# Kernel optimization log

Hardware: AMD Instinct MI355X
Metric: run time of the kernel (lower is better)

The kernel has to match this reference:

```python
import jax, jax.numpy as jnp
from jax import lax
import numpy as np

B, H, W, D_MODEL = 2, 64, 64, 192
D_INNER, D_STATE, DT_RANK = 384, 16, 12
L = H * W
LN_EPS = 1e-5


def setup_inputs() -> dict:
    ks = jax.random.split(jax.random.key(0), 12)
    rng = np.random.default_rng(0)
    perm = rng.permutation(L).astype(np.int32)

    def p(i, shape, scale=0.02):
        return jax.random.normal(ks[i], shape, dtype=jnp.float32) * scale

    return {
        "x": jax.random.normal(ks[0], (B, H, W, D_MODEL), dtype=jnp.float32),
        "condition": jax.random.normal(ks[1], (B, H, W, D_MODEL), dtype=jnp.float32),
        "W_in": p(2, (2 * D_INNER, D_MODEL)),
        "W_con": p(3, (D_INNER, D_MODEL)),
        "conv_w": p(4, (D_INNER, 1, 3, 3)),
        "conv_b": jnp.zeros((D_INNER,), jnp.float32),
        "con_conv_w": p(5, (D_INNER, 1, 3, 3)),
        "con_conv_b": jnp.zeros((D_INNER,), jnp.float32),
        "x_proj_w": p(6, (DT_RANK + 2 * D_STATE, D_INNER)),
        "dt_proj_w": p(7, (D_INNER, DT_RANK)),
        "dt_proj_b": p(8, (D_INNER,), 0.1),
        "A_logs": jnp.tile(jnp.log(jnp.arange(1, D_STATE + 1, dtype=jnp.float32))[None, :], (D_INNER, 1)),
        "Ds": jnp.ones((D_INNER,), jnp.float32),
        "ln_w": jnp.ones((D_INNER,), jnp.float32),
        "ln_b": jnp.zeros((D_INNER,), jnp.float32),
        "W_out": p(9, (D_MODEL, D_INNER)),
        "scan_path": jnp.asarray(perm),
        "rev_scan_path": jnp.asarray(np.argsort(perm).astype(np.int32)),
    }


def _dwconv(x, w, b):
    # depthwise 3x3 conv, SAME padding; x: [B, C, H, W], w: [C, 1, 3, 3]
    y = lax.conv_general_dilated(x, w, (1, 1), "SAME",
                                 dimension_numbers=("NCHW", "OIHW", "NCHW"),
                                 feature_group_count=x.shape[1])
    return y + b[None, :, None, None]


def _selective_scan(u, delta, A, Bs, Cs, D):
    # u, delta: [B, D, L]; A: [D, N]; Bs, Cs: [B, N, L]; D: [D]
    dA = jnp.exp(jnp.einsum("bdl,dn->lbdn", delta, A))          # [L, B, D, N]
    dBu = jnp.einsum("bdl,bnl,bdl->lbdn", delta, Bs, u)          # [L, B, D, N]
    Ct = jnp.transpose(Cs, (2, 0, 1))                             # [L, B, N]
    h0 = jnp.zeros(dA.shape[1:], dA.dtype)

    def step(h, inp):
        a, b, c = inp
        h = a * h + b
        return h, jnp.einsum("bdn,bn->bd", h, c)

    _, ys = lax.scan(step, h0, (dA, dBu, Ct))                     # ys: [L, B, D]
    y = jnp.transpose(ys, (1, 2, 0))                              # [B, D, L]
    return y + u * D[None, :, None]


def _forward(x, condition, W_in, W_con, conv_w, conv_b, con_conv_w, con_conv_b,
             x_proj_w, dt_proj_w, dt_proj_b, A_logs, Ds, ln_w, ln_b, W_out,
             scan_path, rev_scan_path):
    b, h, w, _ = x.shape
    l = h * w
    xz = x @ W_in.T                                               # [B, H, W, 2*Din]
    xa, z = jnp.split(xz, 2, axis=-1)
    z = jax.nn.silu(z)
    c = condition @ W_con.T
    xa = jax.nn.silu(_dwconv(jnp.transpose(xa, (0, 3, 1, 2)), conv_w, conv_b))
    c = jax.nn.silu(_dwconv(jnp.transpose(c, (0, 3, 1, 2)), con_conv_w, con_conv_b))
    d = xa.shape[1]
    xs = xa.reshape(b, d, l)[:, :, scan_path]                     # forward_permutation, K=1
    cs = c.reshape(b, d, l)[:, :, scan_path]
    x_dbl = jnp.einsum("bdl,cd->bcl", xs + cs, x_proj_w)          # [B, R+2N, L]
    r, n = dt_proj_w.shape[1], A_logs.shape[1]
    dts = jnp.einsum("brl,dr->bdl", x_dbl[:, :r], dt_proj_w)
    Bs = x_dbl[:, r:r + n]
    Cs = x_dbl[:, r + n:]
    A = -jnp.exp(A_logs)
    delta = jax.nn.softplus(dts + dt_proj_b[None, :, None])       # delta_softplus=True
    y = _selective_scan(xs, delta, A, Bs, Cs, Ds)                 # [B, D, L]
    y = y[:, :, rev_scan_path]                                    # backward_permutation
    y = jnp.transpose(y, (0, 2, 1))                               # [B, L, D]
    mu = jnp.mean(y, axis=-1, keepdims=True)
    var = jnp.var(y, axis=-1, keepdims=True)
    y = (y - mu) * lax.rsqrt(var + LN_EPS) * ln_w + ln_b          # out_norm
    y = y.reshape(b, h, w, d) * z
    return y @ W_out.T                                            # out_proj (no bias)


def reference(x, condition, W_in, W_con, conv_w, conv_b, con_conv_w, con_conv_b,
              x_proj_w, dt_proj_w, dt_proj_b, A_logs, Ds, ln_w, ln_b, W_out,
              scan_path, rev_scan_path):
    return _forward(x, condition, W_in, W_con, conv_w, conv_b, con_conv_w,
                    con_conv_b, x_proj_w, dt_proj_w, dt_proj_b, A_logs, Ds,
                    ln_w, ln_b, W_out, scan_path, rev_scan_path)
```

## Files before the change

kernel.cpp:

```cpp
#include <hip/hip_runtime.h>
#include <math.h>

#define BB 2
#define HH 64
#define WW 64
#define DM 192
#define DI 384
#define NS 16
#define DTR 12
#define LL 4096
#define ROWS (BB*LL)
#define NCHUNK 64
#define LCHUNK 64
#define NCOMB 448

typedef __attribute__((ext_vector_type(8))) short bf16x8;
typedef __attribute__((ext_vector_type(4))) float f32x4;

__device__ __forceinline__ float silu_f(float v) {
    return v / (1.0f + __expf(-v));
}

__device__ __forceinline__ unsigned short f2bf(float f) {
    union { float f; unsigned int u; } c; c.f = f;
    unsigned int u = c.u;
    u += 0x7fffu + ((u >> 16) & 1u);
    return (unsigned short)(u >> 16);
}

__device__ __forceinline__ bf16x8 f2bf8(float4 a, float4 b) {
    bf16x8 r;
    r[0] = (short)f2bf(a.x); r[1] = (short)f2bf(a.y);
    r[2] = (short)f2bf(a.z); r[3] = (short)f2bf(a.w);
    r[4] = (short)f2bf(b.x); r[5] = (short)f2bf(b.y);
    r[6] = (short)f2bf(b.z); r[7] = (short)f2bf(b.w);
    return r;
}

__global__ __launch_bounds__(256) void prep_weights(
    const float* __restrict__ w_in, const float* __restrict__ w_con,
    const float* __restrict__ w_out,
    const float* __restrict__ x_proj_w, const float* __restrict__ dt_w,
    unsigned short* __restrict__ w_in_bf, unsigned short* __restrict__ w_con_bf,
    unsigned short* __restrict__ w_out_bf, unsigned short* __restrict__ wc)
{
    int idx = blockIdx.x * 256 + threadIdx.x;
    if (idx < 73728) {
        const float4* src; ushort4* dst; int off;
        if (idx < 36864)      { src = (const float4*)w_in;  dst = (ushort4*)w_in_bf;  off = idx; }
        else if (idx < 55296) { src = (const float4*)w_con; dst = (ushort4*)w_con_bf; off = idx - 36864; }
        else                  { src = (const float4*)w_out; dst = (ushort4*)w_out_bf; off = idx - 55296; }
        float4 v = src[off];
        ushort4 o;
        o.x = f2bf(v.x); o.y = f2bf(v.y); o.z = f2bf(v.z); o.w = f2bf(v.w);
        dst[off] = o;
    } else {
        int e = idx - 73728;
        if (e >= NCOMB * DI) return;
        int row = e / DI, k = e - row * DI;
        float v = 0.f;
        if (row < 384) {
            const float* dw = dt_w + row * DTR;
            #pragma unroll
            for (int r = 0; r < DTR; ++r) v += dw[r] * x_proj_w[r * DI + k];
        } else if (row < 416) {
            v = x_proj_w[(12 + (row - 384)) * DI + k];
        }
        wc[e] = f2bf(v);
    }
}

__device__ __forceinline__ void gemm_epilogue(
    int mode, int row, int col, int N, float v,
    const float* __restrict__ bias,
    float* __restrict__ out0, float* __restrict__ out1)
{
    if (mode == 0) {
        if (col < 384) out0[(size_t)row * 384 + col] = v;
        else           out1[(size_t)row * 384 + (col - 384)] = silu_f(v);
    } else if (mode == 1) {
        out0[(size_t)row * N + col] = v;
    } else {
        if (col < 384) {
            float a = v + bias[col];
            out0[(size_t)row * 384 + col] = (a > 20.f) ? a : log1pf(__expf(a));
        } else if (col < 416) {
            int idx = col - 384;
            int pos = (idx < 16) ? ((idx & 7) * 4 + (idx >> 3))
                                 : (((idx - 16) & 7) * 4 + 2 + ((idx - 16) >> 3));
            out1[(size_t)row * 32 + pos] = v;
        }
    }
}

__global__ __launch_bounds__(256) void gemm_bf16(
    const unsigned short* __restrict__ A, const unsigned short* __restrict__ W,
    const float* __restrict__ bias,
    float* __restrict__ out0, float* __restrict__ out1,
    int M, int N, int K, int mode)
{
    __shared__ __align__(16) unsigned short sA[64 * 40];
    __shared__ __align__(16) unsigned short sB[64 * 40];
    const int bm = blockIdx.x * 64;
    const int bn = blockIdx.y * 64;
    const int tid  = threadIdx.x;
    const int wave = tid >> 6;
    const int lane = tid & 63;
    const int quad = lane >> 4;
    const int l16  = lane & 15;
    const int lrow = tid >> 2;
    const int lkof = (tid & 3) * 8;

    f32x4 acc[4];
    #pragma unroll
    for (int t = 0; t < 4; ++t) acc[t] = (f32x4)(0.f);

    const int arow = (wave * 16 + l16) * 40 + quad * 8;

    for (int k0 = 0; k0 < K; k0 += 32) {
        *(bf16x8*)&sA[lrow * 40 + lkof] =
            *(const bf16x8*)&A[(size_t)(bm + lrow) * K + k0 + lkof];
        *(bf16x8*)&sB[lrow * 40 + lkof] =
            *(const bf16x8*)&W[(size_t)(bn + lrow) * K + k0 + lkof];
        __syncthreads();
        bf16x8 a = *(bf16x8*)&sA[arow];
        #pragma unroll
        for (int t = 0; t < 4; ++t) {
            bf16x8 b = *(bf16x8*)&sB[(t * 16 + l16) * 40 + quad * 8];
            acc[t] = __builtin_amdgcn_mfma_f32_16x16x32_bf16(a, b, acc[t], 0, 0, 0);
        }
        __syncthreads();
    }

    #pragma unroll
    for (int t = 0; t < 4; ++t) {
        int col = bn + t * 16 + l16;
        #pragma unroll
        for (int r = 0; r < 4; ++r) {
            int row = bm + wave * 16 + quad * 4 + r;
            gemm_epilogue(mode, row, col, N, acc[t][r], bias, out0, out1);
        }
    }
}

__global__ __launch_bounds__(256) void gemm_dual(
    const float* __restrict__ x, const float* __restrict__ cond,
    const unsigned short* __restrict__ w_in_bf,
    const unsigned short* __restrict__ w_con_bf,
    float* __restrict__ xa_pre, float* __restrict__ z_silu,
    float* __restrict__ c_pre)
{
    const int zz = blockIdx.z;
    if (zz == 1 && blockIdx.y >= 6) return;
    const float* A = zz ? cond : x;
    const unsigned short* W = zz ? w_con_bf : w_in_bf;
    float* out0 = zz ? c_pre : xa_pre;
    float* out1 = z_silu;
    const int mode = zz ? 1 : 0;
    const int N = zz ? 384 : 768;

    __shared__ __align__(16) unsigned short sA[64 * 40];
    __shared__ __align__(16) unsigned short sB[64 * 40];
    const int bm = blockIdx.x * 64;
    const int bn = blockIdx.y * 64;
    const int tid  = threadIdx.x;
    const int wave = tid >> 6;
    const int lane = tid & 63;
    const int quad = lane >> 4;
    const int l16  = lane & 15;
    const int lrow = tid >> 2;
    const int lkof = (tid & 3) * 8;

    f32x4 acc[4];
    #pragma unroll
    for (int t = 0; t < 4; ++t) acc[t] = (f32x4)(0.f);

    const int arow = (wave * 16 + l16) * 40 + quad * 8;

    for (int k0 = 0; k0 < DM; k0 += 32) {
        const float* ap = &A[(size_t)(bm + lrow) * DM + k0 + lkof];
        float4 a0 = *(const float4*)ap;
        float4 a1 = *(const float4*)(ap + 4);
        *(bf16x8*)&sA[lrow * 40 + lkof] = f2bf8(a0, a1);
        *(bf16x8*)&sB[lrow * 40 + lkof] =
            *(const bf16x8*)&W[(size_t)(bn + lrow) * DM + k0 + lkof];
        __syncthreads();
        bf16x8 a = *(bf16x8*)&sA[arow];
        #pragma unroll
        for (int t = 0; t < 4; ++t) {
            bf16x8 b = *(bf16x8*)&sB[(t * 16 + l16) * 40 + quad * 8];
            acc[t] = __builtin_amdgcn_mfma_f32_16x16x32_bf16(a, b, acc[t], 0, 0, 0);
        }
        __syncthreads();
    }

    #pragma unroll
    for (int t = 0; t < 4; ++t) {
        int col = bn + t * 16 + l16;
        #pragma unroll
        for (int r = 0; r < 4; ++r) {
            int row = bm + wave * 16 + quad * 4 + r;
            gemm_epilogue(mode, row, col, N, acc[t][r], nullptr, out0, out1);
        }
    }
}

__global__ __launch_bounds__(256) void dwconv2_scatter(
    const float* __restrict__ xin, const float* __restrict__ cin,
    const float* __restrict__ wx, const float* __restrict__ bx,
    const float* __restrict__ wc, const float* __restrict__ bc,
    const int* __restrict__ rev_scan_path,
    float* __restrict__ xs_buf, unsigned short* __restrict__ s_bf)
{
    const int tile = blockIdx.x;
    const int c0   = blockIdx.y * 64;
    const int b    = blockIdx.z;
    const int h0 = (tile >> 3) * 8, w0 = (tile & 7) * 8;
    __shared__ float smx[10 * 10 * 64];
    __shared__ float smc[10 * 10 * 64];
    __shared__ int   jtile[64];

    for (int idx = threadIdx.x; idx < 6400; idx += 256) {
        int pix = idx >> 6, ch = idx & 63;
        int py = pix / 10, px = pix - py * 10;
        int gh = h0 + py - 1, gw = w0 + px - 1;
        float vx = 0.f, vc = 0.f;
        if (gh >= 0 && gh < 64 && gw >= 0 && gw < 64) {
            size_t g = ((size_t)(b * LL + gh * 64 + gw)) * DI + c0 + ch;
            vx = xin[g]; vc = cin[g];
        }
        smx[idx] = vx; smc[idx] = vc;
    }
    if (threadIdx.x < 64) {
        int l = (h0 + (threadIdx.x >> 3)) * 64 + (w0 + (threadIdx.x & 7));
        jtile[threadIdx.x] = rev_scan_path[l];
    }
    __syncthreads();

    const int ch = threadIdx.x & 63;
    const int pq = threadIdx.x >> 6;
    float wrx[9], wrc[9];
    #pragma unroll
    for (int k = 0; k < 9; ++k) {
        wrx[k] = wx[(c0 + ch) * 9 + k];
        wrc[k] = wc[(c0 + ch) * 9 + k];
    }
    const float bvx = bx[c0 + ch];
    const float bvc = bc[c0 + ch];

    #pragma unroll
    for (int i = 0; i < 16; ++i) {
        int p  = pq * 16 + i;
        int ph = p >> 3, pw = p & 7;
        float ax = bvx, ac = bvc;
        #pragma unroll
        for (int ki = 0; ki < 3; ++ki)
            #pragma unroll
            for (int kj = 0; kj < 3; ++kj) {
                int si = ((ph + ki) * 10 + (pw + kj)) * 64 + ch;
                ax += wrx[ki * 3 + kj] * smx[si];
                ac += wrc[ki * 3 + kj] * smc[si];
            }
        float xv = silu_f(ax);
        float sv = xv + silu_f(ac);
        size_t o = ((size_t)(b * LL + jtile[p])) * DI + c0 + ch;
        xs_buf[o] = xv;
        s_bf[o]   = f2bf(sv);
    }
}

__global__ __launch_bounds__(256) void scan_chunkA(
    const float* __restrict__ xs, const float* __restrict__ delta,
    const float* __restrict__ btct, const float* __restrict__ A_logs,
    float* __restrict__ chunkA, float* __restrict__ chunkB)
{
    const int c = blockIdx.x;
    const int g = blockIdx.y;
    const int b = blockIdx.z;
    const int t = threadIdx.x;
    const int grp = t >> 3, p = t & 7;
    const int d = g * 32 + grp;
    const float Av0 = -__expf(A_logs[d * NS + p]);
    const float Av1 = -__expf(A_logs[d * NS + p + 8]);
    const int j0 = c * LCHUNK;

    const float*  dl = delta + ((size_t)b * LL + j0) * DI + d;
    const float*  ul = xs    + ((size_t)b * LL + j0) * DI + d;
    const float2* bl = (const float2*)btct + ((size_t)b * LL + j0) * 16 + p * 2;

    float h0 = 0.f, h1 = 0.f, Sd = 0.f;
    float dv[4], uv[4]; float2 bv[4];
    #pragma unroll
    for (int q = 0; q < 4; ++q) {
        dv[q] = dl[(size_t)q * DI]; uv[q] = ul[(size_t)q * DI]; bv[q] = bl[(size_t)q * 16];
    }
    for (int j = 0; j < LCHUNK; j += 4) {
        float nd[4], nu[4]; float2 nb[4];
        if (j + 4 < LCHUNK) {
            #pragma unroll
            for (int q = 0; q < 4; ++q) {
                int jj = j + 4 + q;
                nd[q] = dl[(size_t)jj * DI]; nu[q] = ul[(size_t)jj * DI]; nb[q] = bl[(size_t)jj * 16];
            }
        }
        #pragma unroll
        for (int q = 0; q < 4; ++q) {
            float e0 = __expf(dv[q] * Av0);
            float e1 = __expf(dv[q] * Av1);
            float du = dv[q] * uv[q];
            h0 = e0 * h0 + bv[q].x * du;
            h1 = e1 * h1 + bv[q].y * du;
            Sd += dv[q];
        }
        #pragma unroll
        for (int q = 0; q < 4; ++q) { dv[q]=nd[q]; uv[q]=nu[q]; bv[q]=nb[q]; }
    }
    size_t idx = (((size_t)b * DI + d) * 8 + p) * NCHUNK + c;
    ((float2*)chunkA)[idx] = make_float2(__expf(Sd * Av0), __expf(Sd * Av1));
    ((float2*)chunkB)[idx] = make_float2(h0, h1);
}

__global__ __launch_bounds__(256) void scan_combine(
    const float* __restrict__ chunkA, const float* __restrict__ chunkB,
    float* __restrict__ hstart)
{
    const int gid = blockIdx.x * 256 + threadIdx.x;
    const float2* A2 = (const float2*)chunkA + (size_t)gid * NCHUNK;
    const float2* B2 = (const float2*)chunkB + (size_t)gid * NCHUNK;
    float2*       H2 = (float2*)hstart       + (size_t)gid * NCHUNK;
    float h0 = 0.f, h1 = 0.f;
    for (int c = 0; c < NCHUNK; ++c) {
        float2 a = A2[c], bv = B2[c];
        H2[c] = make_float2(h0, h1);
        h0 = a.x * h0 + bv.x;
        h1 = a.y * h1 + bv.y;
    }
}

__global__ __launch_bounds__(256) void scan_chunkC(
    const float* __restrict__ xs, const float* __restrict__ delta,
    const float* __restrict__ btct,
    const float* __restrict__ A_logs, const float* __restrict__ Ds,
    const float* __restrict__ hstart,
    float* __restrict__ yt)
{
    const int c = blockIdx.x;
    const int g = blockIdx.y;
    const int b = blockIdx.z;
    const int t = threadIdx.x;
    const int grp = t >> 3, p = t & 7;
    const int d = g * 32 + grp;
    const float Av0 = -__expf(A_logs[d * NS + p]);
    const float Av1 = -__expf(A_logs[d * NS + p + 8]);
    const float Dv = Ds[d];
    const int j0 = c * LCHUNK;

    const float*  dl  = delta + ((size_t)b * LL + j0) * DI + d;
    const float*  ul  = xs    + ((size_t)b * LL + j0) * DI + d;
    const float4* bcl = (const float4*)btct + ((size_t)b * LL + j0) * 8 + p;
    float* yl = yt + ((size_t)b * LL + j0) * DI + d;

    float2 h = ((const float2*)hstart)[(((size_t)b * DI + d) * 8 + p) * NCHUNK + c];
    float h0 = h.x, h1 = h.y;

    float dv[4], uv[4]; float4 bc[4];
    #pragma unroll
    for (int q = 0; q < 4; ++q) {
        dv[q] = dl[(size_t)q * DI]; uv[q] = ul[(size_t)q * DI]; bc[q] = bcl[(size_t)q * 8];
    }
    for (int j = 0; j < LCHUNK; j += 4) {
        float nd[4], nu[4]; float4 nbc[4];
        if (j + 4 < LCHUNK) {
            #pragma unroll
            for (int q = 0; q < 4; ++q) {
                int jj = j + 4 + q;
                nd[q] = dl[(size_t)jj * DI]; nu[q] = ul[(size_t)jj * DI]; nbc[q] = bcl[(size_t)jj * 8];
            }
        }
        #pragma unroll
        for (int q = 0; q < 4; ++q) {
            float e0 = __expf(dv[q] * Av0);
            float e1 = __expf(dv[q] * Av1);
            float du = dv[q] * uv[q];
            h0 = e0 * h0 + bc[q].x * du;
            h1 = e1 * h1 + bc[q].y * du;
            float acc = h0 * bc[q].z + h1 * bc[q].w;
            acc += __shfl_xor(acc, 4, 8);
            acc += __shfl_xor(acc, 2, 8);
            acc += __shfl_xor(acc, 1, 8);
            if (p == 0) yl[(size_t)(j + q) * DI] = acc + uv[q] * Dv;
        }
        #pragma unroll
        for (int q = 0; q < 4; ++q) { dv[q]=nd[q]; uv[q]=nu[q]; bc[q]=nbc[q]; }
    }
}

__global__ __launch_bounds__(256) void ln_gemm(
    const float* __restrict__ yt, const float* __restrict__ z,
    const int* __restrict__ rev_path,
    const float* __restrict__ ln_w, const float* __restrict__ ln_b,
    const unsigned short* __restrict__ w_out_bf,
    float* __restrict__ out)
{
    __shared__ __align__(16) unsigned short sA[32 * 392];
    __shared__ __align__(16) unsigned short sB[192 * 40];
    const int l0 = blockIdx.x * 32;
    const int tid  = threadIdx.x;
    const int wave = tid >> 6;
    const int lane = tid & 63;

    for (int r = wave; r < 32; r += 4) {
        int gl = l0 + r;
        int b = gl >> 12;
        int pos = gl & (LL - 1);
        int j = b * LL + rev_path[pos];
        const float* yrow = yt + (size_t)j * DI;
        float v[6];
        float s = 0.f, s2 = 0.f;
        #pragma unroll
        for (int i = 0; i < 6; ++i) {
            v[i] = yrow[lane + 64 * i];
            s += v[i]; s2 += v[i] * v[i];
        }
        #pragma unroll
        for (int off = 32; off > 0; off >>= 1) {
            s  += __shfl_xor(s, off);
            s2 += __shfl_xor(s2, off);
        }
        float mu  = s * (1.0f / DI);
        float var = s2 * (1.0f / DI) - mu * mu;
        float inv = rsqrtf(var + 1e-5f);
        const float* zrow = z + (size_t)gl * DI;
        #pragma unroll
        for (int i = 0; i < 6; ++i) {
            int cidx = lane + 64 * i;
            float val = ((v[i] - mu) * inv * ln_w[cidx] + ln_b[cidx]) * zrow[cidx];
            sA[r * 392 + cidx] = f2bf(val);
        }
    }
    __syncthreads();

    const int quad = lane >> 4;
    const int l16  = lane & 15;
    const int wr  = wave >> 1;
    const int wc2 = wave & 1;
    const int r2  = tid >> 2;
    const int kof = (tid & 3) * 8;

    f32x4 acc[6];
    #pragma unroll
    for (int cI = 0; cI < 6; ++cI) acc[cI] = (f32x4)(0.f);

    for (int k0 = 0; k0 < DI; k0 += 32) {
        #pragma unroll
        for (int it = 0; it < 3; ++it) {
            int row = r2 + it * 64;
            *(bf16x8*)&sB[row * 40 + kof] =
                *(const bf16x8*)&w_out_bf[(size_t)row * DI + k0 + kof];
        }
        __syncthreads();
        bf16x8 a = *(bf16x8*)&sA[(wr * 16 + l16) * 392 + k0 + quad * 8];
        #pragma unroll
        for (int cI = 0; cI < 6; ++cI) {
            bf16x8 bb = *(bf16x8*)&sB[(wc2 * 96 + cI * 16 + l16) * 40 + quad * 8];
            acc[cI] = __builtin_amdgcn_mfma_f32_16x16x32_bf16(a, bb, acc[cI], 0, 0, 0);
        }
        __syncthreads();
    }

    #pragma unroll
    for (int cI = 0; cI < 6; ++cI) {
        int col = wc2 * 96 + cI * 16 + l16;
        #pragma unroll
        for (int r = 0; r < 4; ++r) {
            int row = l0 + wr * 16 + quad * 4 + r;
            out[(size_t)row * DM + col] = acc[cI][r];
        }
    }
}

extern "C" void kernel_launch(void* const* d_in, const int* in_sizes, int n_in,
                              void* d_out, int out_size, void* d_ws, size_t ws_size,
                              hipStream_t stream) {
    const float* x          = (const float*)d_in[0];
    const float* cond       = (const float*)d_in[1];
    const float* W_in       = (const float*)d_in[2];
    const float* W_con      = (const float*)d_in[3];
    const float* conv_w     = (const float*)d_in[4];
    const float* conv_b     = (const float*)d_in[5];
    const float* con_conv_w = (const float*)d_in[6];
    const float* con_conv_b = (const float*)d_in[7];
    const float* x_proj_w   = (const float*)d_in[8];
    const float* dt_proj_w  = (const float*)d_in[9];
    const float* dt_proj_b  = (const float*)d_in[10];
    const float* A_logs     = (const float*)d_in[11];
    const float* Ds         = (const float*)d_in[12];
    const float* ln_w       = (const float*)d_in[13];
    const float* ln_b       = (const float*)d_in[14];
    const float* W_out      = (const float*)d_in[15];
    const int*   scan_path  = (const int*)d_in[16];
    const int*   rev_path   = (const int*)d_in[17];
    (void)scan_path;

    float* ws = (float*)d_ws;
    const size_t S  = (size_t)BB * LL * DI;
    const size_t SC = (size_t)NCHUNK * BB * DI * NS;
    float* xa_pre  = ws + 0 * S;
    float* z_silu  = ws + 1 * S;
    float* c_pre   = ws + 2 * S;
    float* xs_buf  = ws + 3 * S;
    float* dl_buf  = ws + 4 * S;
    float* btct    = ws + 5 * S;
    float* chunkA  = btct + (size_t)BB * LL * 32;
    float* chunkB  = chunkA + SC;
    float* hstart  = chunkB + SC;
    float* bfpool  = hstart + SC;

    unsigned short* s_bf     = (unsigned short*)bfpool;
    unsigned short* w_in_bf  = s_bf + (size_t)ROWS * DI;
    unsigned short* w_con_bf = w_in_bf + 768 * DM;
    unsigned short* w_out_bf = w_con_bf + 384 * DM;
    unsigned short* wcomb_bf = w_out_bf + 192 * DI;
    float* yt = xa_pre;

    prep_weights<<<(73728 + NCOMB * DI + 255) / 256, 256, 0, stream>>>(
        W_in, W_con, W_out, x_proj_w, dt_proj_w,
        w_in_bf, w_con_bf, w_out_bf, wcomb_bf);

    gemm_dual<<<dim3(ROWS / 64, 12, 2), 256, 0, stream>>>(
        x, cond, w_in_bf, w_con_bf, xa_pre, z_silu, c_pre);
    dwconv2_scatter<<<dim3(64, 6, BB), 256, 0, stream>>>(
        xa_pre, c_pre, conv_w, conv_b, con_conv_w, con_conv_b,
        rev_path, xs_buf, s_bf);
    gemm_bf16<<<dim3(ROWS / 64, NCOMB / 64), 256, 0, stream>>>(
        s_bf, wcomb_bf, dt_proj_b, dl_buf, btct, ROWS, NCOMB, DI, 2);
    scan_chunkA<<<dim3(NCHUNK, DI / 32, BB), 256, 0, stream>>>(
        xs_buf, dl_buf, btct, A_logs, chunkA, chunkB);
    scan_combine<<<(BB * DI * 8) / 256, 256, 0, stream>>>(chunkA, chunkB, hstart);
    scan_chunkC<<<dim3(NCHUNK, DI / 32, BB), 256, 0, stream>>>(
        xs_buf, dl_buf, btct, A_logs, Ds, hstart, yt);
    ln_gemm<<<ROWS / 32, 256, 0, stream>>>(
        yt, z_silu, rev_path, ln_w, ln_b, w_out_bf, (float*)d_out);
}
```

Before: 238.1 us.

## Split LN+out-proj into LN kernel and generic GEMM, store z as bf16

Splits the fused layernorm+out_proj kernel into a per-row LN/gate kernel that reads contiguous scan rows and scatters them through scan_path to bf16, followed by the generic bf16 GEMM. The SiLU gate z is stored as bf16 to halve its traffic, and the depthwise conv uses 32-channel tiles to launch more blocks. This avoids gathered row reads and the fused kernel's poor occupancy, at the cost of an extra launch and an intermediate bf16 buffer round trip.

New measurement: 231.8 us. -2.6%, faster.

```diff
diff --git a/kernel.cpp b/kernel.cpp
--- a/kernel.cpp
+++ b/kernel.cpp
@@ -26,6 +26,10 @@
     unsigned int u = c.u;
     u += 0x7fffu + ((u >> 16) & 1u);
     return (unsigned short)(u >> 16);
+}
+__device__ __forceinline__ float bf2f(unsigned short h) {
+    union { unsigned int u; float f; } c; c.u = ((unsigned int)h) << 16;
+    return c.f;
 }
 
 __device__ __forceinline__ bf16x8 f2bf8(float4 a, float4 b) {
@@ -73,11 +77,11 @@
 __device__ __forceinline__ void gemm_epilogue(
     int mode, int row, int col, int N, float v,
     const float* __restrict__ bias,
-    float* __restrict__ out0, float* __restrict__ out1)
+    float* __restrict__ out0, void* __restrict__ out1)
 {
     if (mode == 0) {
         if (col < 384) out0[(size_t)row * 384 + col] = v;
-        else           out1[(size_t)row * 384 + (col - 384)] = silu_f(v);
+        else ((unsigned short*)out1)[(size_t)row * 384 + (col - 384)] = f2bf(silu_f(v));
     } else if (mode == 1) {
         out0[(size_t)row * N + col] = v;
     } else {
@@ -88,7 +92,7 @@
             int idx = col - 384;
             int pos = (idx < 16) ? ((idx & 7) * 4 + (idx >> 3))
                                  : (((idx - 16) & 7) * 4 + 2 + ((idx - 16) >> 3));
-            out1[(size_t)row * 32 + pos] = v;
+            ((float*)out1)[(size_t)row * 32 + pos] = v;
         }
     }
 }
@@ -96,7 +100,7 @@
 __global__ __launch_bounds__(256) void gemm_bf16(
     const unsigned short* __restrict__ A, const unsigned short* __restrict__ W,
     const float* __restrict__ bias,
-    float* __restrict__ out0, float* __restrict__ out1,
+    float* __restrict__ out0, void* __restrict__ out1,
     int M, int N, int K, int mode)
 {
     __shared__ __align__(16) unsigned short sA[64 * 40];
@@ -147,7 +151,7 @@
     const float* __restrict__ x, const float* __restrict__ cond,
     const unsigned short* __restrict__ w_in_bf,
     const unsigned short* __restrict__ w_con_bf,
-    float* __restrict__ xa_pre, float* __restrict__ z_silu,
+    float* __restrict__ xa_pre, unsigned short* __restrict__ z_bf,
     float* __restrict__ c_pre)
 {
     const int zz = blockIdx.z;
@@ -155,7 +159,6 @@
     const float* A = zz ? cond : x;
     const unsigned short* W = zz ? w_con_bf : w_in_bf;
     float* out0 = zz ? c_pre : xa_pre;
-    float* out1 = z_silu;
     const int mode = zz ? 1 : 0;
     const int N = zz ? 384 : 768;
 
@@ -200,7 +203,7 @@
         #pragma unroll
         for (int r = 0; r < 4; ++r) {
             int row = bm + wave * 16 + quad * 4 + r;
-            gemm_epilogue(mode, row, col, N, acc[t][r], nullptr, out0, out1);
+            gemm_epilogue(mode, row, col, N, acc[t][r], nullptr, out0, (void*)z_bf);
         }
     }
 }
@@ -213,15 +216,15 @@
     float* __restrict__ xs_buf, unsigned short* __restrict__ s_bf)
 {
     const int tile = blockIdx.x;
-    const int c0   = blockIdx.y * 64;
+    const int c0   = blockIdx.y * 32;
     const int b    = blockIdx.z;
     const int h0 = (tile >> 3) * 8, w0 = (tile & 7) * 8;
-    __shared__ float smx[10 * 10 * 64];
-    __shared__ float smc[10 * 10 * 64];
+    __shared__ float smx[10 * 10 * 32];
+    __shared__ float smc[10 * 10 * 32];
     __shared__ int   jtile[64];
 
-    for (int idx = threadIdx.x; idx < 6400; idx += 256) {
-        int pix = idx >> 6, ch = idx & 63;
+    for (int idx = threadIdx.x; idx < 3200; idx += 256) {
+        int pix = idx >> 5, ch = idx & 31;
         int py = pix / 10, px = pix - py * 10;
         int gh = h0 + py - 1, gw = w0 + px - 1;
         float vx = 0.f, vc = 0.f;
@@ -237,8 +240,8 @@
     }
     __syncthreads();
 
-    const int ch = threadIdx.x & 63;
-    const int pq = threadIdx.x >> 6;
+    const int ch = threadIdx.x & 31;
+    const int pq = threadIdx.x >> 5;
     float wrx[9], wrc[9];
     #pragma unroll
     for (int k = 0; k < 9; ++k) {
@@ -249,15 +252,15 @@
     const float bvc = bc[c0 + ch];
 
     #pragma unroll
-    for (int i = 0; i < 16; ++i) {
-        int p  = pq * 16 + i;
+    for (int i = 0; i < 8; ++i) {
+        int p  = pq * 8 + i;
         int ph = p >> 3, pw = p & 7;
         float ax = bvx, ac = bvc;
         #pragma unroll
         for (int ki = 0; ki < 3; ++ki)
             #pragma unroll
             for (int kj = 0; kj < 3; ++kj) {
-                int si = ((ph + ki) * 10 + (pw + kj)) * 64 + ch;
+                int si = ((ph + ki) * 10 + (pw + kj)) * 32 + ch;
                 ax += wrx[ki * 3 + kj] * smx[si];
                 ac += wrc[ki * 3 + kj] * smc[si];
             }
@@ -395,88 +398,39 @@
     }
 }
 
-__global__ __launch_bounds__(256) void ln_gemm(
-    const float* __restrict__ yt, const float* __restrict__ z,
-    const int* __restrict__ rev_path,
+__global__ __launch_bounds__(128) void ln_mul(
+    const float* __restrict__ yt, const unsigned short* __restrict__ z,
+    const int* __restrict__ scan_path,
     const float* __restrict__ ln_w, const float* __restrict__ ln_b,
-    const unsigned short* __restrict__ w_out_bf,
-    float* __restrict__ out)
-{
-    __shared__ __align__(16) unsigned short sA[32 * 392];
-    __shared__ __align__(16) unsigned short sB[192 * 40];
-    const int l0 = blockIdx.x * 32;
-    const int tid  = threadIdx.x;
-    const int wave = tid >> 6;
-    const int lane = tid & 63;
-
-    for (int r = wave; r < 32; r += 4) {
-        int gl = l0 + r;
-        int b = gl >> 12;
-        int pos = gl & (LL - 1);
-        int j = b * LL + rev_path[pos];
-        const float* yrow = yt + (size_t)j * DI;
-        float v[6];
-        float s = 0.f, s2 = 0.f;
-        #pragma unroll
-        for (int i = 0; i < 6; ++i) {
-            v[i] = yrow[lane + 64 * i];
-            s += v[i]; s2 += v[i] * v[i];
-        }
-        #pragma unroll
-        for (int off = 32; off > 0; off >>= 1) {
-            s  += __shfl_xor(s, off);
-            s2 += __shfl_xor(s2, off);
-        }
-        float mu  = s * (1.0f / DI);
-        float var = s2 * (1.0f / DI) - mu * mu;
-        float inv = rsqrtf(var + 1e-5f);
-        const float* zrow = z + (size_t)gl * DI;
-        #pragma unroll
-        for (int i = 0; i < 6; ++i) {
-            int cidx = lane + 64 * i;
-            float val = ((v[i] - mu) * inv * ln_w[cidx] + ln_b[cidx]) * zrow[cidx];
-            sA[r * 392 + cidx] = f2bf(val);
-        }
-    }
+    unsigned short* __restrict__ yn)
+{
+    const int j = blockIdx.x;
+    const int b = blockIdx.y;
+    const int l = scan_path[j];
+    const int t = threadIdx.x;
+    const float* row = yt + ((size_t)(b * LL + j)) * DI;
+    float v0 = row[t], v1 = row[t + 128], v2 = row[t + 256];
+    float s  = v0 + v1 + v2;
+    float s2 = v0*v0 + v1*v1 + v2*v2;
+    #pragma unroll
+    for (int off = 32; off > 0; off >>= 1) {
+        s  += __shfl_down(s, off);
+        s2 += __shfl_down(s2, off);
+    }
+    __shared__ float red[4];
+    if ((t & 63) == 0) { red[(t >> 6) * 2] = s; red[(t >> 6) * 2 + 1] = s2; }
     __syncthreads();
-
-    const int quad = lane >> 4;
-    const int l16  = lane & 15;
-    const int wr  = wave >> 1;
-    const int wc2 = wave & 1;
-    const int r2  = tid >> 2;
-    const int kof = (tid & 3) * 8;
-
-    f32x4 acc[6];
-    #pragma unroll
-    for (int cI = 0; cI < 6; ++cI) acc[cI] = (f32x4)(0.f);
-
-    for (int k0 = 0; k0 < DI; k0 += 32) {
-        #pragma unroll
-        for (int it = 0; it < 3; ++it) {
-            int row = r2 + it * 64;
-            *(bf16x8*)&sB[row * 40 + kof] =
-                *(const bf16x8*)&w_out_bf[(size_t)row * DI + k0 + kof];
-        }
-        __syncthreads();
-        bf16x8 a = *(bf16x8*)&sA[(wr * 16 + l16) * 392 + k0 + quad * 8];
-        #pragma unroll
-        for (int cI = 0; cI < 6; ++cI) {
-            bf16x8 bb = *(bf16x8*)&sB[(wc2 * 96 + cI * 16 + l16) * 40 + quad * 8];
-            acc[cI] = __builtin_amdgcn_mfma_f32_16x16x32_bf16(a, bb, acc[cI], 0, 0, 0);
-        }
-        __syncthreads();
-    }
-
-    #pragma unroll
-    for (int cI = 0; cI < 6; ++cI) {
-        int col = wc2 * 96 + cI * 16 + l16;
-        #pragma unroll
-        for (int r = 0; r < 4; ++r) {
-            int row = l0 + wr * 16 + quad * 4 + r;
-            out[(size_t)row * DM + col] = acc[cI][r];
-        }
-    }
+    float S  = red[0] + red[2];
+    float S2 = red[1] + red[3];
+    float mu  = S * (1.0f / DI);
+    float var = S2 * (1.0f / DI) - mu * mu;
+    float inv = rsqrtf(var + 1e-5f);
+
+    const unsigned short* zr = z + ((size_t)(b * LL + l)) * DI;
+    unsigned short* o = yn + ((size_t)(b * LL + l)) * DI;
+    o[t]       = f2bf(((v0 - mu) * inv * ln_w[t]       + ln_b[t])       * bf2f(zr[t]));
+    o[t + 128] = f2bf(((v1 - mu) * inv * ln_w[t + 128] + ln_b[t + 128]) * bf2f(zr[t + 128]));
+    o[t + 256] = f2bf(((v2 - mu) * inv * ln_w[t + 256] + ln_b[t + 256]) * bf2f(zr[t + 256]));
 }
 
 extern "C" void kernel_launch(void* const* d_in, const int* in_sizes, int n_in,
@@ -500,13 +454,12 @@
     const float* W_out      = (const float*)d_in[15];
     const int*   scan_path  = (const int*)d_in[16];
     const int*   rev_path   = (const int*)d_in[17];
-    (void)scan_path;
 
     float* ws = (float*)d_ws;
     const size_t S  = (size_t)BB * LL * DI;
     const size_t SC = (size_t)NCHUNK * BB * DI * NS;
     float* xa_pre  = ws + 0 * S;
-    float* z_silu  = ws + 1 * S;
+    float* zslab   = ws + 1 * S;
     float* c_pre   = ws + 2 * S;
     float* xs_buf  = ws + 3 * S;
     float* dl_buf  = ws + 4 * S;
@@ -516,11 +469,13 @@
     float* hstart  = chunkB + SC;
     float* bfpool  = hstart + SC;
 
+    unsigned short* z_bf     = (unsigned short*)zslab;
     unsigned short* s_bf     = (unsigned short*)bfpool;
     unsigned short* w_in_bf  = s_bf + (size_t)ROWS * DI;
     unsigned short* w_con_bf = w_in_bf + 768 * DM;
     unsigned short* w_out_bf = w_con_bf + 384 * DM;
     unsigned short* wcomb_bf = w_out_bf + 192 * DI;
+    unsigned short* yn_bf    = (unsigned short*)c_pre;
     float* yt = xa_pre;
 
     prep_weights<<<(73728 + NCOMB * DI + 255) / 256, 256, 0, stream>>>(
@@ -528,17 +483,18 @@
         w_in_bf, w_con_bf, w_out_bf, wcomb_bf);
 
     gemm_dual<<<dim3(ROWS / 64, 12, 2), 256, 0, stream>>>(
-        x, cond, w_in_bf, w_con_bf, xa_pre, z_silu, c_pre);
-    dwconv2_scatter<<<dim3(64, 6, BB), 256, 0, stream>>>(
+        x, cond, w_in_bf, w_con_bf, xa_pre, z_bf, c_pre);
+    dwconv2_scatter<<<dim3(64, 12, BB), 256, 0, stream>>>(
         xa_pre, c_pre, conv_w, conv_b, con_conv_w, con_conv_b,
         rev_path, xs_buf, s_bf);
     gemm_bf16<<<dim3(ROWS / 64, NCOMB / 64), 256, 0, stream>>>(
-        s_bf, wcomb_bf, dt_proj_b, dl_buf, btct, ROWS, NCOMB, DI, 2);
+        s_bf, wcomb_bf, dt_proj_b, dl_buf, (void*)btct, ROWS, NCOMB, DI, 2);
     scan_chunkA<<<dim3(NCHUNK, DI / 32, BB), 256, 0, stream>>>(
         xs_buf, dl_buf, btct, A_logs, chunkA, chunkB);
     scan_combine<<<(BB * DI * 8) / 256, 256, 0, stream>>>(chunkA, chunkB, hstart);
     scan_chunkC<<<dim3(NCHUNK, DI / 32, BB), 256, 0, stream>>>(
         xs_buf, dl_buf, btct, A_logs, Ds, hstart, yt);
-    ln_gemm<<<ROWS / 32, 256, 0, stream>>>(
-        yt, z_silu, rev_path, ln_w, ln_b, w_out_bf, (float*)d_out);
-}
+    ln_mul<<<dim3(LL, BB), 128, 0, stream>>>(yt, z_bf, scan_path, ln_w, ln_b, yn_bf);
+    gemm_bf16<<<dim3(ROWS / 64, 192 / 64), 256, 0, stream>>>(
+        yn_bf, w_out_bf, nullptr, (float*)d_out, nullptr, ROWS, DM, DI, 1);
+}
```
